# Kernel tuning notes

Measured on AMD Instinct MI355X. Metric: run time of the kernel, lower is better.

Reference implementation:

```python
import jax, jax.numpy as jnp
import numpy as np

D_MODEL = 1024
H = 16
D_K = D_MODEL // H


def setup_inputs() -> dict:
    key = jax.random.key(0)
    ks = jax.random.split(key, 7)
    B, S = 4, 2048
    scale = 1.0 / np.sqrt(D_MODEL)
    return {
        "q": jax.random.normal(ks[0], (B, S, D_MODEL), dtype=jnp.float32),
        "k": jax.random.normal(ks[1], (B, S, D_MODEL), dtype=jnp.float32),
        "v": jax.random.normal(ks[2], (B, S, D_MODEL), dtype=jnp.float32),
        "W_q": jax.random.normal(ks[3], (D_MODEL, D_MODEL), dtype=jnp.float32) * scale,
        "W_k": jax.random.normal(ks[4], (D_MODEL, D_MODEL), dtype=jnp.float32) * scale,
        "W_v": jax.random.normal(ks[5], (D_MODEL, D_MODEL), dtype=jnp.float32) * scale,
        "W_o": jax.random.normal(ks[6], (D_MODEL, D_MODEL), dtype=jnp.float32) * scale,
    }


def reference(q, k, v, W_q, W_k, W_v, W_o):
    B, S, _ = q.shape
    # nn.Linear(bias=False): y = x @ W.T
    def proj(x, W):
        return (x @ W.T).reshape(B, -1, H, D_K).transpose(0, 2, 1, 3)  # [B,H,S,d_k]
    Q = proj(q, W_q)
    K = proj(k, W_k)
    V = proj(v, W_v)
    scores = jnp.einsum('bhqd,bhkd->bhqk', Q, K) / jnp.sqrt(jnp.float32(D_K))
    attn = jax.nn.softmax(scores, axis=-1)  # dropout p=0.0 -> identity
    ctx = jnp.einsum('bhqk,bhkd->bhqd', attn, V)
    ctx = ctx.transpose(0, 2, 1, 3).reshape(B, S, H * D_K)
    return ctx @ W_o.T
```

## Files before the change

### kernel.cpp

```cpp
#include <hip/hip_runtime.h>
#include <stdint.h>


typedef __attribute__((ext_vector_type(8))) short bf16x8;
typedef __attribute__((ext_vector_type(4))) float f32x4;

__device__ __forceinline__ void lds_async16(const void* g, void* l) {
  __builtin_amdgcn_global_load_lds(
      (const __attribute__((address_space(1))) void*)g,
      (__attribute__((address_space(3))) void*)l, 16, 0, 0);
}

__device__ __forceinline__ unsigned short f2bf(float f) {
  union { float f; unsigned u; } v; v.f = f;
  unsigned u = v.u + 0x7fffu + ((v.u >> 16) & 1u);
  return (unsigned short)(u >> 16);
}

__device__ __forceinline__ float fast_exp2(float x) {
#if __has_builtin(__builtin_amdgcn_exp2f)
  return __builtin_amdgcn_exp2f(x);
#else
  return exp2f(x);
#endif
}

__device__ __forceinline__ uint2 pack4(float a, float b, float c, float d) {
#if __has_builtin(__builtin_amdgcn_cvt_pk_bf16_f32)
  typedef __bf16 bf16v2 __attribute__((ext_vector_type(2)));
  union U { bf16v2 v; unsigned u; };
  U x, y;
  x.v = __builtin_amdgcn_cvt_pk_bf16_f32(a, b);
  y.v = __builtin_amdgcn_cvt_pk_bf16_f32(c, d);
  return make_uint2(x.u, y.u);
#else
  return make_uint2((unsigned)f2bf(a) | ((unsigned)f2bf(b) << 16),
                    (unsigned)f2bf(c) | ((unsigned)f2bf(d) << 16));
#endif
}

__global__ void cvt_kernel(const float* s0, const float* s1, const float* s2, const float* s3,
                           unsigned short* d0, unsigned short* d1, unsigned short* d2, unsigned short* d3,
                           int n4) {
  int which = blockIdx.y;
  const float* s = which == 0 ? s0 : which == 1 ? s1 : which == 2 ? s2 : s3;
  unsigned short* d = which == 0 ? d0 : which == 1 ? d1 : which == 2 ? d2 : d3;
  int i = blockIdx.x * 256 + threadIdx.x;
  if (i < n4) {
    float4 v = ((const float4*)s)[i];
    ushort4 o;
    o.x = f2bf(v.x); o.y = f2bf(v.y); o.z = f2bf(v.z); o.w = f2bf(v.w);
    ((ushort4*)d)[i] = o;
  }
}

struct GemmAcc { f32x4 acc[4][4]; };

__device__ __forceinline__ void gemm_core(const unsigned short* __restrict__ Arows,
                                          const unsigned short* __restrict__ Brows,
                                          int tm, int tn, unsigned short* As,
                                          unsigned short* Bs, GemmAcc& g) {
  constexpr int K = 1024;
  const int tid = threadIdx.x;
  const int lane = tid & 63;
  const int wv = tid >> 6;
  const int wm = wv & 1, wn = wv >> 1;
  const int c16 = lane & 15, q4 = lane >> 4;

#pragma unroll
  for (int i = 0; i < 4; ++i)
#pragma unroll
    for (int j = 0; j < 4; ++j)
#pragma unroll
      for (int r = 0; r < 4; ++r) g.acc[i][j][r] = 0.f;

  const int srow = tid >> 3;
  const int gc = (((tid & 7) ^ (srow & 7)) << 3);
  const unsigned short* Arow = Arows + (size_t)(tm * 128 + srow) * K + gc;
  const unsigned short* Brow = Brows + (size_t)(tn * 128 + srow) * K + gc;
  char* AsBase = (char*)As + tid * 16;
  char* BsBase = (char*)Bs + tid * 16;

  for (int k0 = 0; k0 < K; k0 += 64) {
    __syncthreads();
#pragma unroll
    for (int i = 0; i < 4; ++i) {
      lds_async16(Arow + k0 + i * 32 * K, AsBase + i * 4096);
      lds_async16(Brow + k0 + i * 32 * K, BsBase + i * 4096);
    }
    __syncthreads();
#pragma unroll
    for (int ks = 0; ks < 2; ++ks) {
      bf16x8 af[4], bfr[4];
#pragma unroll
      for (int i = 0; i < 4; ++i) {
        int mr = wm * 64 + i * 16 + c16;
        int pa = (ks * 4 + q4) ^ (mr & 7);
        af[i] = *(const bf16x8*)(As + mr * 64 + pa * 8);
        int nr = wn * 64 + i * 16 + c16;
        int pb = (ks * 4 + q4) ^ (nr & 7);
        bfr[i] = *(const bf16x8*)(Bs + nr * 64 + pb * 8);
      }
#pragma unroll
      for (int i = 0; i < 4; ++i)
#pragma unroll
        for (int j = 0; j < 4; ++j)
          g.acc[i][j] = __builtin_amdgcn_mfma_f32_16x16x32_bf16(af[i], bfr[j], g.acc[i][j], 0, 0, 0);
    }
  }
}

__global__ __launch_bounds__(256, 4)
void qkv_kernel(const unsigned short* __restrict__ qb, const unsigned short* __restrict__ kb,
                const unsigned short* __restrict__ vb,
                const unsigned short* __restrict__ wq, const unsigned short* __restrict__ wk,
                const unsigned short* __restrict__ wv_,
                unsigned short* __restrict__ Qb, unsigned short* __restrict__ Kb,
                unsigned short* __restrict__ Vtb) {
  __shared__ unsigned short As[128 * 64];
  __shared__ unsigned short Bs[128 * 64];
  const int z = blockIdx.z;
  const unsigned short* A;
  const unsigned short* B;
  int tm, tn;
  if (z == 0)      { A = qb;  B = wq;  tm = blockIdx.y; tn = blockIdx.x; }
  else if (z == 1) { A = kb;  B = wk;  tm = blockIdx.y; tn = blockIdx.x; }
  else             { A = wv_; B = vb;  tm = blockIdx.x; tn = blockIdx.y; }

  GemmAcc g;
  gemm_core(A, B, tm, tn, As, Bs, g);

  const int lane = threadIdx.x & 63;
  const int wv = threadIdx.x >> 6;
  const int wm = wv & 1, wn = wv >> 1;
  const int c16 = lane & 15, q4 = lane >> 4;
  const float qscale = 0.125f * 1.44269504f;

#pragma unroll
  for (int i = 0; i < 4; ++i)
#pragma unroll
    for (int j = 0; j < 4; ++j)
#pragma unroll
      for (int r = 0; r < 4; ++r) {
        int m = tm * 128 + wm * 64 + i * 16 + q4 * 4 + r;
        int n = tn * 128 + wn * 64 + j * 16 + c16;
        float val = g.acc[i][j][r];
        if (z < 2) {
          if (z == 0) val *= qscale;
          int b = m >> 11, s_ = m & 2047, h = n >> 6, d = n & 63;
          unsigned short* dst = z == 0 ? Qb : Kb;
          dst[(((size_t)(b * 16 + h) * 2048 + s_) << 6) | d] = f2bf(val);
        } else {
          int h = m >> 6, d = m & 63, b = n >> 11, s_ = n & 2047;
          Vtb[((size_t)((b * 16 + h) * 64 + d) << 11) | s_] = f2bf(val);
        }
      }
}

__global__ __launch_bounds__(256, 4)
void out_gemm(const unsigned short* __restrict__ A, const unsigned short* __restrict__ B,
              float* __restrict__ C) {
  __shared__ unsigned short As[128 * 64];
  __shared__ unsigned short Bs[128 * 64];
  GemmAcc g;
  gemm_core(A, B, blockIdx.y, blockIdx.x, As, Bs, g);
  const int lane = threadIdx.x & 63;
  const int wv = threadIdx.x >> 6;
  const int wm = wv & 1, wn = wv >> 1;
  const int c16 = lane & 15, q4 = lane >> 4;
#pragma unroll
  for (int i = 0; i < 4; ++i)
#pragma unroll
    for (int j = 0; j < 4; ++j)
#pragma unroll
      for (int r = 0; r < 4; ++r) {
        int m = blockIdx.y * 128 + wm * 64 + i * 16 + q4 * 4 + r;
        int n = blockIdx.x * 128 + wn * 64 + j * 16 + c16;
        C[(size_t)m * 1024 + n] = g.acc[i][j][r];
      }
}

constexpr int PSS = 136;

__global__ __launch_bounds__(256, 2)
void attn_kernel(const unsigned short* __restrict__ Q,
                 const unsigned short* __restrict__ K,
                 const unsigned short* __restrict__ Vt,
                 unsigned short* __restrict__ ctx) {
  __shared__ unsigned short Ks[128 * 64];
  __shared__ unsigned short Vs[64 * 128];
  __shared__ unsigned short Ps[128 * PSS];

  const int tid = threadIdx.x, lane = tid & 63, w = tid >> 6;
  const int c16 = lane & 15, q4 = lane >> 4;
  const int wbase = w * 32;

  const int idx = blockIdx.x;
  const int slot = idx >> 3;
  const int bh = (idx & 7) * 8 + (slot >> 4);
  const int qt = slot & 15;

  const unsigned short* Qp = Q + ((size_t)bh * 2048 + qt * 128) * 64;
  const unsigned short* Kp = K + (size_t)bh * 2048 * 64;
  const unsigned short* Vp = Vt + (size_t)bh * 64 * 2048;

  const int srow8 = tid >> 3;
  const int gc8 = (((tid & 7) ^ (srow8 & 7)) << 3);

  {
    const unsigned short* Qr = Qp + (size_t)srow8 * 64 + gc8;
    char* base = (char*)Ps + tid * 16;
#pragma unroll
    for (int c = 0; c < 4; ++c) lds_async16(Qr + c * 32 * 64, base + c * 4096);
  }
  __syncthreads();
  bf16x8 qf[2][2];
#pragma unroll
  for (int nn = 0; nn < 2; ++nn)
#pragma unroll
    for (int ks = 0; ks < 2; ++ks) {
      int qr = wbase + nn * 16 + c16;
      int pos = (ks * 4 + q4) ^ (qr & 7);
      qf[nn][ks] = *(const bf16x8*)(Ps + qr * 64 + pos * 8);
    }

  bf16x8 onesf;
  {
    short v = (c16 == 0) ? (short)0x3F80 : (short)0;
#pragma unroll
    for (int j = 0; j < 8; ++j) onesf[j] = v;
  }

  f32x4 oacc[2][4];
  f32x4 lacc[2];
#pragma unroll
  for (int mm = 0; mm < 2; ++mm) {
#pragma unroll
    for (int r = 0; r < 4; ++r) lacc[mm][r] = 0.f;
#pragma unroll
    for (int dj = 0; dj < 4; ++dj)
#pragma unroll
      for (int r = 0; r < 4; ++r) oacc[mm][dj][r] = 0.f;
  }

  const int vrow = tid >> 4;
  const int vslot = tid & 15;
  const int vchunk = vslot ^ (vrow & 15);

  const int ckbase = (q4 >> 1);
  const int ckoff = (q4 & 1) * 4;

  for (int kt = 0; kt < 16; ++kt) {
    __syncthreads();
    {
      const unsigned short* Kr = Kp + ((size_t)kt * 128 + srow8) * 64 + gc8;
      char* base = (char*)Ks + tid * 16;
#pragma unroll
      for (int c = 0; c < 4; ++c) lds_async16(Kr + c * 32 * 64, base + c * 4096);
    }
    {
      const unsigned short* Vr = Vp + (size_t)vrow * 2048 + kt * 128 + vchunk * 8;
      char* base = (char*)Vs + tid * 16;
#pragma unroll
      for (int c = 0; c < 4; ++c) lds_async16(Vr + (size_t)c * 16 * 2048, base + c * 4096);
    }
    __syncthreads();

#pragma unroll
    for (int m = 0; m < 8; ++m) {
      bf16x8 kf0, kf1;
      {
        int row = m * 16 + c16;
        kf0 = *(const bf16x8*)(Ks + row * 64 + ((0 + q4) ^ (row & 7)) * 8);
        kf1 = *(const bf16x8*)(Ks + row * 64 + ((4 + q4) ^ (row & 7)) * 8);
      }
      f32x4 s0 = {0.f, 0.f, 0.f, 0.f}, s1 = {0.f, 0.f, 0.f, 0.f};
      s0 = __builtin_amdgcn_mfma_f32_16x16x32_bf16(kf0, qf[0][0], s0, 0, 0, 0);
      s0 = __builtin_amdgcn_mfma_f32_16x16x32_bf16(kf1, qf[0][1], s0, 0, 0, 0);
      s1 = __builtin_amdgcn_mfma_f32_16x16x32_bf16(kf0, qf[1][0], s1, 0, 0, 0);
      s1 = __builtin_amdgcn_mfma_f32_16x16x32_bf16(kf1, qf[1][1], s1, 0, 0, 0);
      int ck = m * 2 + ckbase;
      {
        int q = wbase + c16;
        *(uint2*)(Ps + q * PSS + ck * 8 + ckoff) =
            pack4(fast_exp2(s0[0]), fast_exp2(s0[1]), fast_exp2(s0[2]), fast_exp2(s0[3]));
      }
      {
        int q = wbase + 16 + c16;
        *(uint2*)(Ps + q * PSS + ck * 8 + ckoff) =
            pack4(fast_exp2(s1[0]), fast_exp2(s1[1]), fast_exp2(s1[2]), fast_exp2(s1[3]));
      }
    }

#pragma unroll
    for (int ks2 = 0; ks2 < 4; ++ks2) {
      bf16x8 vf[4];
#pragma unroll
      for (int dj = 0; dj < 4; ++dj) {
        int dr = dj * 16 + c16;
        int pos = (ks2 * 4 + q4) ^ (dr & 15);
        vf[dj] = *(const bf16x8*)(Vs + dr * 128 + pos * 8);
      }
      bf16x8 pf[2];
#pragma unroll
      for (int mm = 0; mm < 2; ++mm) {
        int qr = wbase + mm * 16 + c16;
        pf[mm] = *(const bf16x8*)(Ps + qr * PSS + (ks2 * 4 + q4) * 8);
      }
#pragma unroll
      for (int mm = 0; mm < 2; ++mm) {
        lacc[mm] = __builtin_amdgcn_mfma_f32_16x16x32_bf16(pf[mm], onesf, lacc[mm], 0, 0, 0);
#pragma unroll
        for (int dj = 0; dj < 4; ++dj)
          oacc[mm][dj] = __builtin_amdgcn_mfma_f32_16x16x32_bf16(pf[mm], vf[dj], oacc[mm][dj], 0, 0, 0);
      }
    }
  }

  int b = bh >> 4, h = bh & 15;
#pragma unroll
  for (int mm = 0; mm < 2; ++mm)
#pragma unroll
    for (int r = 0; r < 4; ++r) {
      float l = __shfl(lacc[mm][r], lane & 48, 64);
      float inv = 1.f / l;
      int s_ = qt * 128 + wbase + mm * 16 + q4 * 4 + r;
#pragma unroll
      for (int dj = 0; dj < 4; ++dj) {
        int d = dj * 16 + c16;
        ctx[((size_t)(b * 2048 + s_)) * 1024 + h * 64 + d] = f2bf(oacc[mm][dj][r] * inv);
      }
    }
}

extern "C" void kernel_launch(void* const* d_in, const int* in_sizes, int n_in,
                              void* d_out, int out_size, void* d_ws, size_t ws_size,
                              hipStream_t stream) {
  const float* q  = (const float*)d_in[0];
  const float* k  = (const float*)d_in[1];
  const float* v  = (const float*)d_in[2];
  const float* Wq = (const float*)d_in[3];
  const float* Wk = (const float*)d_in[4];
  const float* Wv = (const float*)d_in[5];
  const float* Wo = (const float*)d_in[6];

  char* ws = (char*)d_ws;
  unsigned short* qb  = (unsigned short*)(ws);
  unsigned short* kb  = (unsigned short*)(ws + (16u << 20));
  unsigned short* vb  = (unsigned short*)(ws + (32u << 20));
  unsigned short* wqb = (unsigned short*)(ws + (48u << 20));
  unsigned short* wkb = (unsigned short*)(ws + (50u << 20));
  unsigned short* wvb = (unsigned short*)(ws + (52u << 20));
  unsigned short* wob = (unsigned short*)(ws + (54u << 20));
  unsigned short* Qb  = (unsigned short*)(ws + (56u << 20));
  unsigned short* Kb  = (unsigned short*)(ws + (72u << 20));
  unsigned short* Vtb = (unsigned short*)(ws + (88u << 20));
  unsigned short* ctxb = qb;

  cvt_kernel<<<dim3(1024, 4), 256, 0, stream>>>(Wq, Wk, Wv, Wo, wqb, wkb, wvb, wob, 262144);
  cvt_kernel<<<dim3(8192, 3), 256, 0, stream>>>(q, k, v, q, qb, kb, vb, qb, 2097152);

  qkv_kernel<<<dim3(8, 64, 3), 256, 0, stream>>>(qb, kb, vb, wqb, wkb, wvb, Qb, Kb, Vtb);

  attn_kernel<<<dim3(1024), 256, 0, stream>>>(Qb, Kb, Vtb, ctxb);

  out_gemm<<<dim3(8, 64), 256, 0, stream>>>(ctxb, wob, (float*)d_out);
}
```

Measured before the change: 346.9 us.

## Fuse fp32-to-bf16 activation conversion into QKV GEMM and prefetch K/V in registers

Removes the separate activation conversion kernel by having the QKV projection GEMM load fp32 inputs directly, convert them to bf16 in registers and store them to LDS, with a one-step register prefetch. The attention kernel replaces direct global-to-LDS loads of K/V tiles with register prefetching of the next tile, and precomputes LDS addresses. Launch bounds are relaxed to allow more registers. This aims to cut a full pass of memory traffic, at the cost of doubled global read width in the GEMM and higher register pressure.

```diff
diff --git a/kernel.cpp b/kernel.cpp
--- a/kernel.cpp
+++ b/kernel.cpp
@@ -39,6 +39,12 @@
 #endif
 }
 
+__device__ __forceinline__ void cvt8_store(float4 a, float4 b, void* dst) {
+  uint2 lo = pack4(a.x, a.y, a.z, a.w);
+  uint2 hi = pack4(b.x, b.y, b.z, b.w);
+  *(uint4*)dst = make_uint4(lo.x, lo.y, hi.x, hi.y);
+}
+
 __global__ void cvt_kernel(const float* s0, const float* s1, const float* s2, const float* s3,
                            unsigned short* d0, unsigned short* d1, unsigned short* d2, unsigned short* d3,
                            int n4) {
@@ -56,10 +62,10 @@
 
 struct GemmAcc { f32x4 acc[4][4]; };
 
-__device__ __forceinline__ void gemm_core(const unsigned short* __restrict__ Arows,
-                                          const unsigned short* __restrict__ Brows,
-                                          int tm, int tn, unsigned short* As,
-                                          unsigned short* Bs, GemmAcc& g) {
+template <bool AF, bool BF>
+__device__ __forceinline__ void gemm_core2(const void* Ap, const void* Bp,
+                                           int tm, int tn, unsigned short* As,
+                                           unsigned short* Bs, GemmAcc& g) {
   constexpr int K = 1024;
   const int tid = threadIdx.x;
   const int lane = tid & 63;
@@ -76,19 +82,60 @@
 
   const int srow = tid >> 3;
   const int gc = (((tid & 7) ^ (srow & 7)) << 3);
-  const unsigned short* Arow = Arows + (size_t)(tm * 128 + srow) * K + gc;
-  const unsigned short* Brow = Brows + (size_t)(tn * 128 + srow) * K + gc;
+  const unsigned short* Arow16 = (const unsigned short*)Ap + (size_t)(tm * 128 + srow) * K + gc;
+  const unsigned short* Brow16 = (const unsigned short*)Bp + (size_t)(tn * 128 + srow) * K + gc;
+  const float* Arow32 = (const float*)Ap + (size_t)(tm * 128 + srow) * K + gc;
+  const float* Brow32 = (const float*)Bp + (size_t)(tn * 128 + srow) * K + gc;
   char* AsBase = (char*)As + tid * 16;
   char* BsBase = (char*)Bs + tid * 16;
 
+  float4 pre[8];
+  if (AF) {
+#pragma unroll
+    for (int i = 0; i < 4; ++i) {
+      pre[2 * i]     = *(const float4*)(Arow32 + i * 32 * K);
+      pre[2 * i + 1] = *(const float4*)(Arow32 + i * 32 * K + 4);
+    }
+  }
+  if (BF) {
+#pragma unroll
+    for (int i = 0; i < 4; ++i) {
+      pre[2 * i]     = *(const float4*)(Brow32 + i * 32 * K);
+      pre[2 * i + 1] = *(const float4*)(Brow32 + i * 32 * K + 4);
+    }
+  }
+
   for (int k0 = 0; k0 < K; k0 += 64) {
     __syncthreads();
-#pragma unroll
-    for (int i = 0; i < 4; ++i) {
-      lds_async16(Arow + k0 + i * 32 * K, AsBase + i * 4096);
-      lds_async16(Brow + k0 + i * 32 * K, BsBase + i * 4096);
+    if (AF) {
+#pragma unroll
+      for (int i = 0; i < 4; ++i) cvt8_store(pre[2 * i], pre[2 * i + 1], AsBase + i * 4096);
+    } else {
+#pragma unroll
+      for (int i = 0; i < 4; ++i) lds_async16(Arow16 + k0 + i * 32 * K, AsBase + i * 4096);
+    }
+    if (BF) {
+#pragma unroll
+      for (int i = 0; i < 4; ++i) cvt8_store(pre[2 * i], pre[2 * i + 1], BsBase + i * 4096);
+    } else {
+#pragma unroll
+      for (int i = 0; i < 4; ++i) lds_async16(Brow16 + k0 + i * 32 * K, BsBase + i * 4096);
     }
     __syncthreads();
+    if (AF && k0 + 64 < K) {
+#pragma unroll
+      for (int i = 0; i < 4; ++i) {
+        pre[2 * i]     = *(const float4*)(Arow32 + k0 + 64 + i * 32 * K);
+        pre[2 * i + 1] = *(const float4*)(Arow32 + k0 + 64 + i * 32 * K + 4);
+      }
+    }
+    if (BF && k0 + 64 < K) {
+#pragma unroll
+      for (int i = 0; i < 4; ++i) {
+        pre[2 * i]     = *(const float4*)(Brow32 + k0 + 64 + i * 32 * K);
+        pre[2 * i + 1] = *(const float4*)(Brow32 + k0 + 64 + i * 32 * K + 4);
+      }
+    }
 #pragma unroll
     for (int ks = 0; ks < 2; ++ks) {
       bf16x8 af[4], bfr[4];
@@ -110,9 +157,9 @@
   }
 }
 
-__global__ __launch_bounds__(256, 4)
-void qkv_kernel(const unsigned short* __restrict__ qb, const unsigned short* __restrict__ kb,
-                const unsigned short* __restrict__ vb,
+__global__ __launch_bounds__(256, 2)
+void qkv_kernel(const float* __restrict__ qf, const float* __restrict__ kf,
+                const float* __restrict__ vf,
                 const unsigned short* __restrict__ wq, const unsigned short* __restrict__ wk,
                 const unsigned short* __restrict__ wv_,
                 unsigned short* __restrict__ Qb, unsigned short* __restrict__ Kb,
@@ -120,15 +167,18 @@
   __shared__ unsigned short As[128 * 64];
   __shared__ unsigned short Bs[128 * 64];
   const int z = blockIdx.z;
-  const unsigned short* A;
-  const unsigned short* B;
   int tm, tn;
-  if (z == 0)      { A = qb;  B = wq;  tm = blockIdx.y; tn = blockIdx.x; }
-  else if (z == 1) { A = kb;  B = wk;  tm = blockIdx.y; tn = blockIdx.x; }
-  else             { A = wv_; B = vb;  tm = blockIdx.x; tn = blockIdx.y; }
-
   GemmAcc g;
-  gemm_core(A, B, tm, tn, As, Bs, g);
+  if (z == 0) {
+    tm = blockIdx.y; tn = blockIdx.x;
+    gemm_core2<true, false>(qf, wq, tm, tn, As, Bs, g);
+  } else if (z == 1) {
+    tm = blockIdx.y; tn = blockIdx.x;
+    gemm_core2<true, false>(kf, wk, tm, tn, As, Bs, g);
+  } else {
+    tm = blockIdx.x; tn = blockIdx.y;
+    gemm_core2<false, true>(wv_, vf, tm, tn, As, Bs, g);
+  }
 
   const int lane = threadIdx.x & 63;
   const int wv = threadIdx.x >> 6;
@@ -157,13 +207,13 @@
       }
 }
 
-__global__ __launch_bounds__(256, 4)
+__global__ __launch_bounds__(256, 2)
 void out_gemm(const unsigned short* __restrict__ A, const unsigned short* __restrict__ B,
               float* __restrict__ C) {
   __shared__ unsigned short As[128 * 64];
   __shared__ unsigned short Bs[128 * 64];
   GemmAcc g;
-  gemm_core(A, B, blockIdx.y, blockIdx.x, As, Bs, g);
+  gemm_core2<false, false>(A, B, blockIdx.y, blockIdx.x, As, Bs, g);
   const int lane = threadIdx.x & 63;
   const int wv = threadIdx.x >> 6;
   const int wm = wv & 1, wn = wv >> 1;
@@ -207,13 +257,25 @@
   const int srow8 = tid >> 3;
   const int gc8 = (((tid & 7) ^ (srow8 & 7)) << 3);
 
+  const unsigned short* Kr = Kp + (size_t)srow8 * 64 + gc8;
+  const int vrow = tid >> 4;
+  const int vchunk = (tid & 15) ^ (vrow & 15);
+  const unsigned short* Vr = Vp + (size_t)vrow * 2048 + vchunk * 8;
+
   {
     const unsigned short* Qr = Qp + (size_t)srow8 * 64 + gc8;
     char* base = (char*)Ps + tid * 16;
 #pragma unroll
     for (int c = 0; c < 4; ++c) lds_async16(Qr + c * 32 * 64, base + c * 4096);
   }
+  uint4 kpre[4], vpre[4];
+#pragma unroll
+  for (int c = 0; c < 4; ++c) {
+    kpre[c] = *(const uint4*)(Kr + c * 2048);
+    vpre[c] = *(const uint4*)(Vr + c * 32768);
+  }
   __syncthreads();
+
   bf16x8 qf[2][2];
 #pragma unroll
   for (int nn = 0; nn < 2; ++nn)
@@ -243,76 +305,64 @@
       for (int r = 0; r < 4; ++r) oacc[mm][dj][r] = 0.f;
   }
 
-  const int vrow = tid >> 4;
-  const int vslot = tid & 15;
-  const int vchunk = vslot ^ (vrow & 15);
-
-  const int ckbase = (q4 >> 1);
-  const int ckoff = (q4 & 1) * 4;
+  const unsigned short* kb0 = Ks + c16 * 64 + ((q4 ^ (c16 & 7)) * 8);
+  const unsigned short* kb1 = Ks + c16 * 64 + (((4 + q4) ^ (c16 & 7)) * 8);
+  const unsigned short* vb_[4];
+#pragma unroll
+  for (int ks2 = 0; ks2 < 4; ++ks2)
+    vb_[ks2] = Vs + c16 * 128 + (((ks2 * 4 + q4) ^ c16) * 8);
+  const unsigned short* pb[4];
+#pragma unroll
+  for (int ks2 = 0; ks2 < 4; ++ks2)
+    pb[ks2] = Ps + (wbase + c16) * PSS + (ks2 * 4 + q4) * 8;
+  unsigned short* pw0 = Ps + (wbase + c16) * PSS + (q4 >> 1) * 8 + (q4 & 1) * 4;
+  unsigned short* pw1 = pw0 + 16 * PSS;
 
   for (int kt = 0; kt < 16; ++kt) {
     __syncthreads();
+#pragma unroll
+    for (int c = 0; c < 4; ++c) {
+      *(uint4*)((char*)Ks + tid * 16 + c * 4096) = kpre[c];
+      *(uint4*)((char*)Vs + tid * 16 + c * 4096) = vpre[c];
+    }
+    __syncthreads();
     {
-      const unsigned short* Kr = Kp + ((size_t)kt * 128 + srow8) * 64 + gc8;
-      char* base = (char*)Ks + tid * 16;
-#pragma unroll
-      for (int c = 0; c < 4; ++c) lds_async16(Kr + c * 32 * 64, base + c * 4096);
-    }
-    {
-      const unsigned short* Vr = Vp + (size_t)vrow * 2048 + kt * 128 + vchunk * 8;
-      char* base = (char*)Vs + tid * 16;
-#pragma unroll
-      for (int c = 0; c < 4; ++c) lds_async16(Vr + (size_t)c * 16 * 2048, base + c * 4096);
-    }
-    __syncthreads();
+      int ktn = (kt < 15) ? kt + 1 : 15;
+#pragma unroll
+      for (int c = 0; c < 4; ++c) {
+        kpre[c] = *(const uint4*)(Kr + (size_t)ktn * 8192 + c * 2048);
+        vpre[c] = *(const uint4*)(Vr + (size_t)ktn * 128 + c * 32768);
+      }
+    }
 
 #pragma unroll
     for (int m = 0; m < 8; ++m) {
-      bf16x8 kf0, kf1;
-      {
-        int row = m * 16 + c16;
-        kf0 = *(const bf16x8*)(Ks + row * 64 + ((0 + q4) ^ (row & 7)) * 8);
-        kf1 = *(const bf16x8*)(Ks + row * 64 + ((4 + q4) ^ (row & 7)) * 8);
-      }
+      bf16x8 kf0 = *(const bf16x8*)(kb0 + m * 1024);
+      bf16x8 kf1 = *(const bf16x8*)(kb1 + m * 1024);
       f32x4 s0 = {0.f, 0.f, 0.f, 0.f}, s1 = {0.f, 0.f, 0.f, 0.f};
       s0 = __builtin_amdgcn_mfma_f32_16x16x32_bf16(kf0, qf[0][0], s0, 0, 0, 0);
       s0 = __builtin_amdgcn_mfma_f32_16x16x32_bf16(kf1, qf[0][1], s0, 0, 0, 0);
       s1 = __builtin_amdgcn_mfma_f32_16x16x32_bf16(kf0, qf[1][0], s1, 0, 0, 0);
       s1 = __builtin_amdgcn_mfma_f32_16x16x32_bf16(kf1, qf[1][1], s1, 0, 0, 0);
-      int ck = m * 2 + ckbase;
-      {
-        int q = wbase + c16;
-        *(uint2*)(Ps + q * PSS + ck * 8 + ckoff) =
-            pack4(fast_exp2(s0[0]), fast_exp2(s0[1]), fast_exp2(s0[2]), fast_exp2(s0[3]));
-      }
-      {
-        int q = wbase + 16 + c16;
-        *(uint2*)(Ps + q * PSS + ck * 8 + ckoff) =
-            pack4(fast_exp2(s1[0]), fast_exp2(s1[1]), fast_exp2(s1[2]), fast_exp2(s1[3]));
-      }
+      *(uint2*)(pw0 + m * 16) =
+          pack4(fast_exp2(s0[0]), fast_exp2(s0[1]), fast_exp2(s0[2]), fast_exp2(s0[3]));
+      *(uint2*)(pw1 + m * 16) =
+          pack4(fast_exp2(s1[0]), fast_exp2(s1[1]), fast_exp2(s1[2]), fast_exp2(s1[3]));
     }
 
 #pragma unroll
     for (int ks2 = 0; ks2 < 4; ++ks2) {
-      bf16x8 vf[4];
+      bf16x8 vfr[4];
+#pragma unroll
+      for (int dj = 0; dj < 4; ++dj) vfr[dj] = *(const bf16x8*)(vb_[ks2] + dj * 2048);
+      bf16x8 pf0 = *(const bf16x8*)(pb[ks2]);
+      bf16x8 pf1 = *(const bf16x8*)(pb[ks2] + 16 * PSS);
+      lacc[0] = __builtin_amdgcn_mfma_f32_16x16x32_bf16(pf0, onesf, lacc[0], 0, 0, 0);
+      lacc[1] = __builtin_amdgcn_mfma_f32_16x16x32_bf16(pf1, onesf, lacc[1], 0, 0, 0);
 #pragma unroll
       for (int dj = 0; dj < 4; ++dj) {
-        int dr = dj * 16 + c16;
-        int pos = (ks2 * 4 + q4) ^ (dr & 15);
-        vf[dj] = *(const bf16x8*)(Vs + dr * 128 + pos * 8);
-      }
-      bf16x8 pf[2];
-#pragma unroll
-      for (int mm = 0; mm < 2; ++mm) {
-        int qr = wbase + mm * 16 + c16;
-        pf[mm] = *(const bf16x8*)(Ps + qr * PSS + (ks2 * 4 + q4) * 8);
-      }
-#pragma unroll
-      for (int mm = 0; mm < 2; ++mm) {
-        lacc[mm] = __builtin_amdgcn_mfma_f32_16x16x32_bf16(pf[mm], onesf, lacc[mm], 0, 0, 0);
-#pragma unroll
-        for (int dj = 0; dj < 4; ++dj)
-          oacc[mm][dj] = __builtin_amdgcn_mfma_f32_16x16x32_bf16(pf[mm], vf[dj], oacc[mm][dj], 0, 0, 0);
+        oacc[0][dj] = __builtin_amdgcn_mfma_f32_16x16x32_bf16(pf0, vfr[dj], oacc[0][dj], 0, 0, 0);
+        oacc[1][dj] = __builtin_amdgcn_mfma_f32_16x16x32_bf16(pf1, vfr[dj], oacc[1][dj], 0, 0, 0);
       }
     }
   }
@@ -345,22 +395,18 @@
   const float* Wo = (const float*)d_in[6];
 
   char* ws = (char*)d_ws;
-  unsigned short* qb  = (unsigned short*)(ws);
-  unsigned short* kb  = (unsigned short*)(ws + (16u << 20));
-  unsigned short* vb  = (unsigned short*)(ws + (32u << 20));
-  unsigned short* wqb = (unsigned short*)(ws + (48u << 20));
-  unsigned short* wkb = (unsigned short*)(ws + (50u << 20));
-  unsigned short* wvb = (unsigned short*)(ws + (52u << 20));
-  unsigned short* wob = (unsigned short*)(ws + (54u << 20));
-  unsigned short* Qb  = (unsigned short*)(ws + (56u << 20));
-  unsigned short* Kb  = (unsigned short*)(ws + (72u << 20));
-  unsigned short* Vtb = (unsigned short*)(ws + (88u << 20));
-  unsigned short* ctxb = qb;
+  unsigned short* ctxb = (unsigned short*)(ws);
+  unsigned short* wqb  = (unsigned short*)(ws + (48u << 20));
+  unsigned short* wkb  = (unsigned short*)(ws + (50u << 20));
+  unsigned short* wvb  = (unsigned short*)(ws + (52u << 20));
+  unsigned short* wob  = (unsigned short*)(ws + (54u << 20));
+  unsigned short* Qb   = (unsigned short*)(ws + (56u << 20));
+  unsigned short* Kb   = (unsigned short*)(ws + (72u << 20));
+  unsigned short* Vtb  = (unsigned short*)(ws + (88u << 20));
 
   cvt_kernel<<<dim3(1024, 4), 256, 0, stream>>>(Wq, Wk, Wv, Wo, wqb, wkb, wvb, wob, 262144);
-  cvt_kernel<<<dim3(8192, 3), 256, 0, stream>>>(q, k, v, q, qb, kb, vb, qb, 2097152);
-
-  qkv_kernel<<<dim3(8, 64, 3), 256, 0, stream>>>(qb, kb, vb, wqb, wkb, wvb, Qb, Kb, Vtb);
+
+  qkv_kernel<<<dim3(8, 64, 3), 256, 0, stream>>>(q, k, v, wqb, wkb, wvb, Qb, Kb, Vtb);
 
   attn_kernel<<<dim3(1024), 256, 0, stream>>>(Qb, Kb, Vtb, ctxb);
 
```

Result: slower. 430.9 us (+24.2%).

## Double-buffer K/V tiles in attention with smaller key tiles and higher occupancy

Applied to the files above, without the earlier changes.

The attention kernel now processes 64-key tiles instead of 128 and double-buffers K and V in LDS. The next tile's async loads are issued before computing the current one, leaving a single barrier per iteration. The P staging buffer shrinks (PSS 72), so the attention launch bound rises to 3 blocks per SM, while the GEMM kernels drop to 2 blocks, which frees registers. The gain depends on whether the async loads have completed at the trailing barrier; the loop relies on that barrier without an explicit wait on the load counter, which is a correctness risk.

```diff
diff --git a/kernel.cpp b/kernel.cpp
--- a/kernel.cpp
+++ b/kernel.cpp
@@ -110,7 +110,7 @@
   }
 }
 
-__global__ __launch_bounds__(256, 4)
+__global__ __launch_bounds__(256, 2)
 void qkv_kernel(const unsigned short* __restrict__ qb, const unsigned short* __restrict__ kb,
                 const unsigned short* __restrict__ vb,
                 const unsigned short* __restrict__ wq, const unsigned short* __restrict__ wk,
@@ -157,7 +157,7 @@
       }
 }
 
-__global__ __launch_bounds__(256, 4)
+__global__ __launch_bounds__(256, 2)
 void out_gemm(const unsigned short* __restrict__ A, const unsigned short* __restrict__ B,
               float* __restrict__ C) {
   __shared__ unsigned short As[128 * 64];
@@ -180,15 +180,15 @@
       }
 }
 
-constexpr int PSS = 136;
-
-__global__ __launch_bounds__(256, 2)
+constexpr int PSS = 72;
+
+__global__ __launch_bounds__(256, 3)
 void attn_kernel(const unsigned short* __restrict__ Q,
                  const unsigned short* __restrict__ K,
                  const unsigned short* __restrict__ Vt,
                  unsigned short* __restrict__ ctx) {
-  __shared__ unsigned short Ks[128 * 64];
-  __shared__ unsigned short Vs[64 * 128];
+  __shared__ unsigned short Ks[2][64 * 64];
+  __shared__ unsigned short Vs[2][64 * 64];
   __shared__ unsigned short Ps[128 * PSS];
 
   const int tid = threadIdx.x, lane = tid & 63, w = tid >> 6;
@@ -207,13 +207,24 @@
   const int srow8 = tid >> 3;
   const int gc8 = (((tid & 7) ^ (srow8 & 7)) << 3);
 
+  const unsigned short* Krs = Kp + (size_t)srow8 * 64 + gc8;
+  const unsigned short* Vrs = Vp + (size_t)srow8 * 2048 + gc8;
+  char* KdBase = (char*)&Ks[0][0] + tid * 16;
+  char* VdBase = (char*)&Vs[0][0] + tid * 16;
+
   {
     const unsigned short* Qr = Qp + (size_t)srow8 * 64 + gc8;
     char* base = (char*)Ps + tid * 16;
 #pragma unroll
     for (int c = 0; c < 4; ++c) lds_async16(Qr + c * 32 * 64, base + c * 4096);
   }
+#pragma unroll
+  for (int c = 0; c < 2; ++c) {
+    lds_async16(Krs + c * 2048, KdBase + c * 4096);
+    lds_async16(Vrs + c * 65536, VdBase + c * 4096);
+  }
   __syncthreads();
+
   bf16x8 qf[2][2];
 #pragma unroll
   for (int nn = 0; nn < 2; ++nn)
@@ -223,6 +234,7 @@
       int pos = (ks * 4 + q4) ^ (qr & 7);
       qf[nn][ks] = *(const bf16x8*)(Ps + qr * 64 + pos * 8);
     }
+  __syncthreads();
 
   bf16x8 onesf;
   {
@@ -243,78 +255,62 @@
       for (int r = 0; r < 4; ++r) oacc[mm][dj][r] = 0.f;
   }
 
-  const int vrow = tid >> 4;
-  const int vslot = tid & 15;
-  const int vchunk = vslot ^ (vrow & 15);
-
-  const int ckbase = (q4 >> 1);
-  const int ckoff = (q4 & 1) * 4;
-
-  for (int kt = 0; kt < 16; ++kt) {
-    __syncthreads();
-    {
-      const unsigned short* Kr = Kp + ((size_t)kt * 128 + srow8) * 64 + gc8;
-      char* base = (char*)Ks + tid * 16;
-#pragma unroll
-      for (int c = 0; c < 4; ++c) lds_async16(Kr + c * 32 * 64, base + c * 4096);
-    }
-    {
-      const unsigned short* Vr = Vp + (size_t)vrow * 2048 + kt * 128 + vchunk * 8;
-      char* base = (char*)Vs + tid * 16;
-#pragma unroll
-      for (int c = 0; c < 4; ++c) lds_async16(Vr + (size_t)c * 16 * 2048, base + c * 4096);
-    }
-    __syncthreads();
-
-#pragma unroll
-    for (int m = 0; m < 8; ++m) {
-      bf16x8 kf0, kf1;
-      {
-        int row = m * 16 + c16;
-        kf0 = *(const bf16x8*)(Ks + row * 64 + ((0 + q4) ^ (row & 7)) * 8);
-        kf1 = *(const bf16x8*)(Ks + row * 64 + ((4 + q4) ^ (row & 7)) * 8);
-      }
+  const int kb0 = c16 * 64 + ((q4 ^ (c16 & 7)) * 8);
+  const int kb1 = c16 * 64 + (((4 + q4) ^ (c16 & 7)) * 8);
+  int vbo[2];
+#pragma unroll
+  for (int ks2 = 0; ks2 < 2; ++ks2)
+    vbo[ks2] = c16 * 64 + (((ks2 * 4 + q4) ^ (c16 & 7)) * 8);
+  const unsigned short* pb0 = Ps + (wbase + c16) * PSS + q4 * 8;
+  unsigned short* pw0 = Ps + (wbase + c16) * PSS + q4 * 4;
+  unsigned short* pw1 = pw0 + 16 * PSS;
+
+  for (int kt = 0; kt < 32; ++kt) {
+    const unsigned short* KsC = &Ks[kt & 1][0];
+    const unsigned short* VsC = &Vs[kt & 1][0];
+    if (kt < 31) {
+      int nb = (kt + 1) & 1;
+      size_t ko = (size_t)(kt + 1) * 4096;
+      size_t vo = (size_t)(kt + 1) * 64;
+#pragma unroll
+      for (int c = 0; c < 2; ++c) {
+        lds_async16(Krs + ko + c * 2048, KdBase + nb * 8192 + c * 4096);
+        lds_async16(Vrs + vo + c * 65536, VdBase + nb * 8192 + c * 4096);
+      }
+    }
+
+#pragma unroll
+    for (int m = 0; m < 4; ++m) {
+      bf16x8 kf0 = *(const bf16x8*)(KsC + kb0 + m * 1024);
+      bf16x8 kf1 = *(const bf16x8*)(KsC + kb1 + m * 1024);
       f32x4 s0 = {0.f, 0.f, 0.f, 0.f}, s1 = {0.f, 0.f, 0.f, 0.f};
       s0 = __builtin_amdgcn_mfma_f32_16x16x32_bf16(kf0, qf[0][0], s0, 0, 0, 0);
       s0 = __builtin_amdgcn_mfma_f32_16x16x32_bf16(kf1, qf[0][1], s0, 0, 0, 0);
       s1 = __builtin_amdgcn_mfma_f32_16x16x32_bf16(kf0, qf[1][0], s1, 0, 0, 0);
       s1 = __builtin_amdgcn_mfma_f32_16x16x32_bf16(kf1, qf[1][1], s1, 0, 0, 0);
-      int ck = m * 2 + ckbase;
-      {
-        int q = wbase + c16;
-        *(uint2*)(Ps + q * PSS + ck * 8 + ckoff) =
-            pack4(fast_exp2(s0[0]), fast_exp2(s0[1]), fast_exp2(s0[2]), fast_exp2(s0[3]));
-      }
-      {
-        int q = wbase + 16 + c16;
-        *(uint2*)(Ps + q * PSS + ck * 8 + ckoff) =
-            pack4(fast_exp2(s1[0]), fast_exp2(s1[1]), fast_exp2(s1[2]), fast_exp2(s1[3]));
-      }
-    }
-
-#pragma unroll
-    for (int ks2 = 0; ks2 < 4; ++ks2) {
-      bf16x8 vf[4];
+      *(uint2*)(pw0 + m * 16) =
+          pack4(fast_exp2(s0[0]), fast_exp2(s0[1]), fast_exp2(s0[2]), fast_exp2(s0[3]));
+      *(uint2*)(pw1 + m * 16) =
+          pack4(fast_exp2(s1[0]), fast_exp2(s1[1]), fast_exp2(s1[2]), fast_exp2(s1[3]));
+    }
+
+#pragma unroll
+    for (int ks2 = 0; ks2 < 2; ++ks2) {
+      bf16x8 vfr[4];
+#pragma unroll
+      for (int dj = 0; dj < 4; ++dj) vfr[dj] = *(const bf16x8*)(VsC + vbo[ks2] + dj * 1024);
+      bf16x8 pf0 = *(const bf16x8*)(pb0 + ks2 * 32);
+      bf16x8 pf1 = *(const bf16x8*)(pb0 + ks2 * 32 + 16 * PSS);
+      lacc[0] = __builtin_amdgcn_mfma_f32_16x16x32_bf16(pf0, onesf, lacc[0], 0, 0, 0);
+      lacc[1] = __builtin_amdgcn_mfma_f32_16x16x32_bf16(pf1, onesf, lacc[1], 0, 0, 0);
 #pragma unroll
       for (int dj = 0; dj < 4; ++dj) {
-        int dr = dj * 16 + c16;
-        int pos = (ks2 * 4 + q4) ^ (dr & 15);
-        vf[dj] = *(const bf16x8*)(Vs + dr * 128 + pos * 8);
-      }
-      bf16x8 pf[2];
-#pragma unroll
-      for (int mm = 0; mm < 2; ++mm) {
-        int qr = wbase + mm * 16 + c16;
-        pf[mm] = *(const bf16x8*)(Ps + qr * PSS + (ks2 * 4 + q4) * 8);
-      }
-#pragma unroll
-      for (int mm = 0; mm < 2; ++mm) {
-        lacc[mm] = __builtin_amdgcn_mfma_f32_16x16x32_bf16(pf[mm], onesf, lacc[mm], 0, 0, 0);
-#pragma unroll
-        for (int dj = 0; dj < 4; ++dj)
-          oacc[mm][dj] = __builtin_amdgcn_mfma_f32_16x16x32_bf16(pf[mm], vf[dj], oacc[mm][dj], 0, 0, 0);
-      }
-    }
+        oacc[0][dj] = __builtin_amdgcn_mfma_f32_16x16x32_bf16(pf0, vfr[dj], oacc[0][dj], 0, 0, 0);
+        oacc[1][dj] = __builtin_amdgcn_mfma_f32_16x16x32_bf16(pf1, vfr[dj], oacc[1][dj], 0, 0, 0);
+      }
+    }
+
+    __syncthreads();
   }
 
   int b = bh >> 4, h = bh & 15;
```

Result: no change. 343.8 us (-0.9%).
